# Optimization experiments

Hardware: AMD Instinct MI355X
Metric: run time of the kernel (lower is better)

The kernel has to match this reference:

```python
import jax, jax.numpy as jnp
import numpy as np
import math

N = 100000
E = 1600000
IN_DIM = 64
OUT_DIM = 64
EPS = 1e-5


def setup_inputs() -> dict:
    key = jax.random.key(0)
    ks = jax.random.split(key, 12)
    s = 1.0 / math.sqrt(IN_DIM)
    inp = {
        "geo_x": jax.random.normal(ks[0], (N, IN_DIM), dtype=jnp.float32),
        "euc_x": jax.random.normal(ks[1], (N, IN_DIM), dtype=jnp.float32),
        "Wq": jax.random.uniform(ks[2], (OUT_DIM, IN_DIM), minval=-s, maxval=s, dtype=jnp.float32),
        "bq": jnp.zeros((OUT_DIM,), jnp.float32),
        "Wk": jax.random.uniform(ks[3], (OUT_DIM, IN_DIM), minval=-s, maxval=s, dtype=jnp.float32),
        "bk": jnp.zeros((OUT_DIM,), jnp.float32),
        "Wv": jax.random.uniform(ks[4], (OUT_DIM, IN_DIM), minval=-s, maxval=s, dtype=jnp.float32),
        "bv": jnp.zeros((OUT_DIM,), jnp.float32),
        "Wskip": jax.random.uniform(ks[5], (OUT_DIM, IN_DIM), minval=-s, maxval=s, dtype=jnp.float32),
        "bskip": jnp.zeros((OUT_DIM,), jnp.float32),
        "ln_w": jnp.ones((OUT_DIM,), jnp.float32),
        "ln_b": jnp.zeros((OUT_DIM,), jnp.float32),
        "edge_index": jax.random.randint(ks[6], (2, E), 0, N, dtype=jnp.int64),
    }
    return inp


def reference(geo_x, euc_x, Wq, bq, Wk, bk, Wv, bv, Wskip, bskip, ln_w, ln_b, edge_index):
    n = euc_x.shape[0]
    src, dst = edge_index[0], edge_index[1]

    # TransformerConv, heads=1: q from target (euc), k/v from source (geo)
    q = euc_x @ Wq.T + bq                      # [N, C]
    k = geo_x @ Wk.T + bk                      # [N, C]
    v = geo_x @ Wv.T + bv                      # [N, C]
    C = q.shape[-1]

    # per-edge attention logits
    alpha = jnp.sum(q[dst] * k[src], axis=-1) / math.sqrt(C)   # [E]

    # segment softmax over incoming edges of each destination node
    amax = jax.ops.segment_max(alpha, dst, num_segments=n)
    amax = jnp.where(jnp.isfinite(amax), amax, 0.0)
    ex = jnp.exp(alpha - amax[dst])
    denom = jax.ops.segment_sum(ex, dst, num_segments=n)
    w = ex / (denom[dst] + 1e-16)                              # [E]

    # scatter-aggregate weighted values + root (skip) transform
    agg = jax.ops.segment_sum(w[:, None] * v[src], dst, num_segments=n)  # [N, C]
    out = agg + euc_x @ Wskip.T + bskip

    # PyG LayerNorm, mode='graph', batch=None: normalize over all nodes+channels
    mean = out.mean()
    xc = out - mean
    std = jnp.sqrt(jnp.mean(xc * xc))
    out = xc / (std + EPS) * ln_w + ln_b

    return jax.nn.relu(out)
```

## Files before the change

kernel.cpp:

```cpp
#include <hip/hip_runtime.h>
#include <hip/hip_fp16.h>


using short8 = __attribute__((ext_vector_type(8))) short;
using f32x4  = __attribute__((ext_vector_type(4))) float;
using h2     = __attribute__((ext_vector_type(2))) _Float16;
using u32x4  = __attribute__((ext_vector_type(4))) unsigned;
using u32x2  = __attribute__((ext_vector_type(2))) unsigned;
using f32x4v = __attribute__((ext_vector_type(4))) float;

#define QSCALE 31.75f
#define VDESC  0.031496062992f
#define SCI    1.7889250e-4f

#define CAP   4608
#define NCBMAX 400

__device__ inline int ntload(const int* p) {
    return __builtin_nontemporal_load(p);
}
__device__ inline unsigned ntload(const unsigned* p) {
    return __builtin_nontemporal_load(p);
}
__device__ inline uint2 ntload(const uint2* p) {
    u32x2 v = __builtin_nontemporal_load((const u32x2*)p);
    return make_uint2(v.x, v.y);
}
__device__ inline uint4 ntload(const uint4* p) {
    u32x4 v = __builtin_nontemporal_load((const u32x4*)p);
    return make_uint4(v.x, v.y, v.z, v.w);
}
__device__ inline float4 ntload(const float4* p) {
    f32x4v v = __builtin_nontemporal_load((const f32x4v*)p);
    return make_float4(v.x, v.y, v.z, v.w);
}
__device__ inline void ntstore(unsigned* p, unsigned v) {
    __builtin_nontemporal_store(v, p);
}
__device__ inline void ntstore(uint4* p, uint4 v) {
    u32x4 t; t.x = v.x; t.y = v.y; t.z = v.z; t.w = v.w;
    __builtin_nontemporal_store(t, (u32x4*)p);
}
__device__ inline void ntstore(float4* p, float4 v) {
    f32x4v t; t.x = v.x; t.y = v.y; t.z = v.z; t.w = v.w;
    __builtin_nontemporal_store(t, (f32x4v*)p);
}

__device__ inline unsigned short f2bf(float f) {
    unsigned u = __float_as_uint(f);
    unsigned r = u + 0x7FFFu + ((u >> 16) & 1u);
    return (unsigned short)(r >> 16);
}
__device__ inline unsigned short f2h(float f) {
    union { _Float16 h; unsigned short u; } c;
    c.h = (_Float16)f;
    return c.u;
}
__device__ inline h2 u2h2(unsigned u) {
    union { unsigned u; h2 h; } c; c.u = u; return c.h;
}
__device__ inline signed char f2i8(float f) {
    float v = f * QSCALE;
    v = fminf(fmaxf(v, -127.f), 127.f);
    return (signed char)__float2int_rn(v);
}

__device__ inline float fexp2(float x) {
#if __has_builtin(__builtin_amdgcn_exp2f)
    return __builtin_amdgcn_exp2f(x);
#else
    return __expf(x * 0.6931471805599453f);
#endif
}

__device__ inline int dot8i(uint2 q, uint2 k) {
#if __has_builtin(__builtin_amdgcn_sdot4)
    int t = __builtin_amdgcn_sdot4((int)q.x, (int)k.x, 0, false);
    return  __builtin_amdgcn_sdot4((int)q.y, (int)k.y, t, false);
#else
    int t = 0;
    #pragma unroll
    for (int i = 0; i < 4; ++i) {
        int qa = (int)(q.x << (24 - 8 * i)) >> 24;
        int ka = (int)(k.x << (24 - 8 * i)) >> 24;
        int qb = (int)(q.y << (24 - 8 * i)) >> 24;
        int kb = (int)(k.y << (24 - 8 * i)) >> 24;
        t += qa * ka + qb * kb;
    }
    return t;
#endif
}

__global__ __launch_bounds__(256) void k0_wconv(
    const float* __restrict__ Wq, const float* __restrict__ Wk,
    const float* __restrict__ Wv, const float* __restrict__ Wsk,
    unsigned short* __restrict__ wbf, int* __restrict__ zbase, int zcount)
{
    if (blockIdx.x == 16) {
        for (int i = threadIdx.x; i < zcount; i += 256) zbase[i] = 0;
        return;
    }
    int mat = blockIdx.x >> 2;
    int i4  = (blockIdx.x & 3) * 256 + threadIdx.x;
    const float* W = (mat == 0) ? Wq : (mat == 1) ? Wk : (mat == 2) ? Wv : Wsk;
    float4 w = *(const float4*)(W + (long)i4 * 4);
    ushort4 o;
    o.x = f2bf(w.x); o.y = f2bf(w.y); o.z = f2bf(w.z); o.w = f2bf(w.w);
    *(ushort4*)(wbf + (long)mat * 4096 + (long)i4 * 4) = o;
}

__global__ __launch_bounds__(256, 4) void k1_proj(
    const float* __restrict__ geo, const float* __restrict__ euc,
    const unsigned short* __restrict__ wbf,
    const float* __restrict__ bq, const float* __restrict__ bk,
    const float* __restrict__ bv, const float* __restrict__ bsk,
    signed char* __restrict__ q8b, signed char* __restrict__ kv8,
    unsigned short* __restrict__ skb, int N)
{
    __shared__ __align__(16) char smem[2 * 64 * 208];
    const int tid  = threadIdx.x;
    const int lane = tid & 63;
    const int w    = tid >> 6;
    const int qq   = lane >> 4;
    const int m    = lane & 15;
    const long base = (long)blockIdx.x * 128;

    char* t0 = smem;
    char* t1 = smem + 64 * 208;

    const long nodeA0 = base + w * 16 + m;
    const long nodeA1 = base + 64 + w * 16 + m;

    auto loadA = [&](const float* __restrict__ x, long node, short8 a[2]) {
        const float* px = x + node * 64;
        const bool v = (node < N);
        #pragma unroll
        for (int kh = 0; kh < 2; ++kh) {
            float4 f0 = v ? ntload((const float4*)(px + kh * 32 + qq * 8))
                          : make_float4(0.f, 0.f, 0.f, 0.f);
            float4 f1 = v ? ntload((const float4*)(px + kh * 32 + qq * 8 + 4))
                          : make_float4(0.f, 0.f, 0.f, 0.f);
            short8 r;
            r[0] = (short)f2bf(f0.x); r[1] = (short)f2bf(f0.y);
            r[2] = (short)f2bf(f0.z); r[3] = (short)f2bf(f0.w);
            r[4] = (short)f2bf(f1.x); r[5] = (short)f2bf(f1.y);
            r[6] = (short)f2bf(f1.z); r[7] = (short)f2bf(f1.w);
            a[kh] = r;
        }
    };
    auto loadB = [&](int mat, short8 b[2][4]) {
        #pragma unroll
        for (int kh = 0; kh < 2; ++kh)
            #pragma unroll
            for (int nt = 0; nt < 4; ++nt)
                b[kh][nt] = *(const short8*)(wbf + (long)mat * 4096 +
                                             (nt * 16 + m) * 64 + kh * 32 + qq * 8);
    };
    auto mmul = [&](const short8 a[2], const short8 b[2][4], f32x4 acc[4]) {
        #pragma unroll
        for (int nt = 0; nt < 4; ++nt) acc[nt] = (f32x4)(0.f);
        #pragma unroll
        for (int kh = 0; kh < 2; ++kh)
            #pragma unroll
            for (int nt = 0; nt < 4; ++nt)
                acc[nt] = __builtin_amdgcn_mfma_f32_16x16x32_bf16(a[kh], b[kh][nt], acc[nt], 0, 0, 0);
    };

    auto emit_i8 = [&](const f32x4 acc[4], const float* __restrict__ bias, char* tile) {
        #pragma unroll
        for (int nt = 0; nt < 4; ++nt) {
            int c = nt * 16 + m;
            float bs = bias[c];
            #pragma unroll
            for (int r = 0; r < 4; ++r) {
                int nl = w * 16 + qq * 4 + r;
                *(signed char*)(tile + nl * 208 + c) = f2i8(acc[nt][r] + bs);
            }
        }
    };
    auto emit_h = [&](const f32x4 acc[4], const float* __restrict__ bias, char* tile) {
        #pragma unroll
        for (int nt = 0; nt < 4; ++nt) {
            int c = nt * 16 + m;
            float bs = bias[c];
            #pragma unroll
            for (int r = 0; r < 4; ++r) {
                int nl = w * 16 + qq * 4 + r;
                *(unsigned short*)(tile + nl * 208 + 64 + c * 2) = f2h(acc[nt][r] + bs);
            }
        }
    };
    auto emit_kv = [&](const f32x4 acc[4], const float* __restrict__ bias,
                       char* tile, int vpart) {
        #pragma unroll
        for (int nt = 0; nt < 4; ++nt) {
            int c = nt * 16 + m;
            float bs = bias[c];
            int boff = (c >> 3) * 16 + vpart * 8 + (c & 7);
            #pragma unroll
            for (int r = 0; r < 4; ++r) {
                int nl = w * 16 + qq * 4 + r;
                *(signed char*)(tile + nl * 208 + boff) = f2i8(acc[nt][r] + bs);
            }
        }
    };

    short8 a0[2], a1[2];
    short8 B[2][4];
    f32x4 acc[4];

    loadA(euc, nodeA0, a0);
    loadA(euc, nodeA1, a1);
    loadB(0, B);
    mmul(a0, B, acc); emit_i8(acc, bq, t0);
    mmul(a1, B, acc); emit_i8(acc, bq, t1);
    loadB(3, B);
    mmul(a0, B, acc); emit_h(acc, bsk, t0);
    mmul(a1, B, acc); emit_h(acc, bsk, t1);
    __syncthreads();
    #pragma unroll
    for (int t = 0; t < 2; ++t) {
        const char* te = t ? t1 : t0;
        const long tb = base + t * 64;
        {
            int n = tid >> 2, j = tid & 3;
            long nd = tb + n;
            if (nd < N)
                *(int4*)(q8b + nd * 64 + j * 16) = *(const int4*)(te + n * 208 + j * 16);
        }
        #pragma unroll
        for (int it = 0; it < 2; ++it) {
            int idx = it * 256 + tid;
            int n = idx >> 3, j = idx & 7;
            long nd = tb + n;
            if (nd < N)
                *(int4*)((char*)skb + nd * 128 + j * 16) =
                    *(const int4*)(te + n * 208 + 64 + j * 16);
        }
    }
    __syncthreads();

    loadA(geo, nodeA0, a0);
    loadA(geo, nodeA1, a1);
    loadB(1, B);
    mmul(a0, B, acc); emit_kv(acc, bk, t0, 0);
    mmul(a1, B, acc); emit_kv(acc, bk, t1, 0);
    loadB(2, B);
    mmul(a0, B, acc); emit_kv(acc, bv, t0, 1);
    mmul(a1, B, acc); emit_kv(acc, bv, t1, 1);
    __syncthreads();
    #pragma unroll
    for (int t = 0; t < 2; ++t) {
        const char* tg = t ? t1 : t0;
        const long tb = base + t * 64;
        #pragma unroll
        for (int it = 0; it < 2; ++it) {
            int idx = it * 256 + tid;
            int n = idx >> 3, j = idx & 7;
            long nd = tb + n;
            if (nd < N)
                *(int4*)(kv8 + nd * 128 + j * 16) = *(const int4*)(tg + n * 208 + j * 16);
        }
    }
}

__global__ __launch_bounds__(512) void k2a_part(
    const int* __restrict__ ei, int E, int N,
    int* __restrict__ ccur, unsigned* __restrict__ tmp)
{
    __shared__ unsigned ebuf[4096];
    __shared__ unsigned short cbuf[4096];
    __shared__ int h[NCBMAX], offA[NCBMAX], lc[NCBMAX], creg[NCBMAX];
    __shared__ int sc[512];

    const int tid = threadIdx.x;
    const int NCB = (N + 255) >> 8;
    const long e0 = (long)blockIdx.x * 4096;
    const int tileN = (int)(((long)E - e0 < 4096) ? ((long)E - e0) : 4096);

    for (int i = tid; i < NCB; i += 512) { h[i] = 0; lc[i] = 0; }
    __syncthreads();

    const int* srcp = ei;
    const int* dstp = ei + E;
    unsigned wj[8];
    int cbj[8];
    #pragma unroll
    for (int j = 0; j < 8; ++j) {
        int i = j * 512 + tid;
        wj[j] = 0u; cbj[j] = -1;
        if (i < tileN) {
            int d = ntload(&dstp[e0 + i]), s = ntload(&srcp[e0 + i]);
            cbj[j] = d >> 8;
            wj[j]  = ((unsigned)(d & 255) << 17) | (unsigned)s;
            atomicAdd(&h[cbj[j]], 1);
        }
    }
    __syncthreads();

    sc[tid] = (tid < NCB) ? h[tid] : 0;
    __syncthreads();
    int own = sc[tid];
    for (int off = 1; off < 512; off <<= 1) {
        int v = (tid >= off) ? sc[tid - off] : 0;
        __syncthreads();
        sc[tid] += v;
        __syncthreads();
    }
    if (tid < NCB) offA[tid] = sc[tid] - own;
    if (tid < NCB && h[tid] > 0)
        creg[tid] = atomicAdd(&ccur[tid], h[tid]);
    __syncthreads();

    #pragma unroll
    for (int j = 0; j < 8; ++j) {
        if (cbj[j] >= 0) {
            int pos = offA[cbj[j]] + atomicAdd(&lc[cbj[j]], 1);
            ebuf[pos] = wj[j];
            cbuf[pos] = (unsigned short)cbj[j];
        }
    }
    __syncthreads();

    #pragma unroll
    for (int j = 0; j < 8; ++j) {
        int i = j * 512 + tid;
        if (i < tileN) {
            int cb = cbuf[i];
            int r  = creg[cb] + (i - offA[cb]);
            if (r < CAP) ntstore(&tmp[(long)cb * CAP + r], ebuf[i]);
        }
    }
}

__global__ __launch_bounds__(256, 8) void k3_attn(
    const signed char* __restrict__ q8b, const signed char* __restrict__ kv8,
    const unsigned short* __restrict__ skb,
    const int* __restrict__ ccnt, const unsigned* __restrict__ tmp,
    unsigned short* __restrict__ preb,
    float* __restrict__ partS, float* __restrict__ partSS, int N)
{
    __shared__ unsigned bkt[64 * 65];
    __shared__ int dcnt[64];
    __shared__ unsigned char perm[64];
    __shared__ float redS[4], redSS[4];
    const int tid  = threadIdx.x;
    const int lane = tid & 63;
    const int w    = tid >> 6;
    const int g0   = tid >> 3;
    const int gl   = tid & 7;
    const int bin  = blockIdx.x;
    const int cb   = bin >> 2;
    const unsigned sub = (unsigned)(bin & 3);
    const long nodeBase = (long)bin * 64;

    if (tid < 64) dcnt[tid] = 0;
    __syncthreads();

    int len = ccnt[cb];
    if (len > CAP) len = CAP;
    const unsigned* reg = tmp + (long)cb * CAP;
    for (int e = tid; e < len; e += 256) {
        unsigned wv = ntload(&reg[e]);
        if (((wv >> 23) & 3u) == sub) {
            int d = (wv >> 17) & 63;
            int slot = atomicAdd(&dcnt[d], 1);
            if (slot < 64) bkt[d * 65 + slot] = wv & 0x1FFFFu;
        }
    }
    __syncthreads();

    if (tid < 64) {
        int d = dcnt[tid]; if (d > 64) d = 64;
        int r = 0;
        for (int j = 0; j < 64; ++j) {
            int dj = dcnt[j]; if (dj > 64) dj = 64;
            r += (dj > d) || ((dj == d) && (j < tid));
        }
        perm[r] = (unsigned char)tid;
    }
    __syncthreads();

    float sacc = 0.f, ssacc = 0.f;

    for (int half = 0; half < 2; ++half) {
        const int row  = perm[half ? (63 - g0) : g0];
        const long node = nodeBase + row;

        uint2 qu = make_uint2(0, 0);
        if (node < N) qu = ntload((const uint2*)(q8b + node * 64 + gl * 8));

        int deg = dcnt[row];
        if (deg > 64) deg = 64;

        float den = 0.f;
        float a0=0.f,a1=0.f,a2=0.f,a3=0.f,a4=0.f,a5=0.f,a6=0.f,a7=0.f;

        auto vacc = [&](unsigned vx, unsigned vy, float ex) {
            a0 = fmaf((float)((int)(vx << 24) >> 24), ex, a0);
            a1 = fmaf((float)((int)(vx << 16) >> 24), ex, a1);
            a2 = fmaf((float)((int)(vx <<  8) >> 24), ex, a2);
            a3 = fmaf((float)((int)(vx      ) >> 24), ex, a3);
            a4 = fmaf((float)((int)(vy << 24) >> 24), ex, a4);
            a5 = fmaf((float)((int)(vy << 16) >> 24), ex, a5);
            a6 = fmaf((float)((int)(vy <<  8) >> 24), ex, a6);
            a7 = fmaf((float)((int)(vy      ) >> 24), ex, a7);
        };

        if (deg > 0) {
            const int rb  = row * 65;
            const int dm1 = deg - 1;
            auto ld = [&](int i) -> uint4 {
                int ii = (i < deg) ? i : dm1;
                unsigned s = bkt[rb + ii];
                return *(const uint4*)(kv8 + (long)s * 128 + gl * 16);
            };
            auto body = [&](uint4 r, int e) {
                int t = dot8i(qu, make_uint2(r.x, r.y));
                t += __shfl_xor(t, 1);
                t += __shfl_xor(t, 2);
                t += __shfl_xor(t, 4);
                float ex = (e < deg) ? fexp2((float)t * SCI) : 0.f;
                den += ex;
                vacc(r.z, r.w, ex);
            };

            uint4 r0 = ld(0), r1 = ld(1), r2 = ld(2), r3 = ld(3);
            for (int s = 0; s < deg; s += 4) {
                body(r0, s);     r0 = ld(s + 4);
                body(r1, s + 1); r1 = ld(s + 5);
                body(r2, s + 2); r2 = ld(s + 6);
                body(r3, s + 3); r3 = ld(s + 7);
            }
        }

        if (node < N) {
            float inv = VDESC / (den + 1e-16f);
            uint4 sk = ntload((const uint4*)((const char*)skb + node * 128 + gl * 16));
            h2 s0 = u2h2(sk.x), s1 = u2h2(sk.y), s2 = u2h2(sk.z), s3 = u2h2(sk.w);
            float o0 = a0 * inv + (float)s0.x, o1 = a1 * inv + (float)s0.y;
            float o2 = a2 * inv + (float)s1.x, o3 = a3 * inv + (float)s1.y;
            float o4 = a4 * inv + (float)s2.x, o5 = a5 * inv + (float)s2.y;
            float o6 = a6 * inv + (float)s3.x, o7 = a7 * inv + (float)s3.y;
            uint4 ov;
            ov.x = (unsigned)f2h(o0) | ((unsigned)f2h(o1) << 16);
            ov.y = (unsigned)f2h(o2) | ((unsigned)f2h(o3) << 16);
            ov.z = (unsigned)f2h(o4) | ((unsigned)f2h(o5) << 16);
            ov.w = (unsigned)f2h(o6) | ((unsigned)f2h(o7) << 16);
            ntstore((uint4*)((char*)preb + node * 128 + gl * 16), ov);
            sacc  += (o0 + o1 + o2 + o3) + (o4 + o5 + o6 + o7);
            ssacc += o0*o0 + o1*o1 + o2*o2 + o3*o3 + o4*o4 + o5*o5 + o6*o6 + o7*o7;
        }
    }

    #pragma unroll
    for (int m = 1; m <= 32; m <<= 1) {
        sacc  += __shfl_xor(sacc, m);
        ssacc += __shfl_xor(ssacc, m);
    }
    if (lane == 0) { redS[w] = sacc; redSS[w] = ssacc; }
    __syncthreads();
    if (tid == 0) {
        float s = 0.f, ss = 0.f;
        #pragma unroll
        for (int i = 0; i < 4; ++i) { s += redS[i]; ss += redSS[i]; }
        partS[bin]  = s;
        partSS[bin] = ss;
    }
}

__global__ __launch_bounds__(256) void k35_stats(
    const float* __restrict__ partS, const float* __restrict__ partSS,
    int nparts, float* __restrict__ stats, float M)
{
    __shared__ float rs[256], rss[256];
    float s = 0.f, ss = 0.f;
    for (int i = threadIdx.x; i < nparts; i += 256) { s += partS[i]; ss += partSS[i]; }
    rs[threadIdx.x] = s; rss[threadIdx.x] = ss;
    __syncthreads();
    for (int st = 128; st > 0; st >>= 1) {
        if (threadIdx.x < st) {
            rs[threadIdx.x]  += rs[threadIdx.x + st];
            rss[threadIdx.x] += rss[threadIdx.x + st];
        }
        __syncthreads();
    }
    if (threadIdx.x == 0) {
        float mean = rs[0] / M;
        float var  = rss[0] / M - mean * mean;
        if (var < 0.f) var = 0.f;
        stats[0] = mean;
        stats[1] = 1.f / (sqrtf(var) + 1e-5f);
    }
}

__global__ __launch_bounds__(256) void k4_ln(
    const unsigned short* __restrict__ preb, float* __restrict__ out,
    const float* __restrict__ lnw, const float* __restrict__ lnb,
    const float* __restrict__ stats, int M8)
{
    int i = blockIdx.x * 256 + threadIdx.x;
    if (i >= M8) return;
    float mean = stats[0], scale = stats[1];
    uint4 pv = ntload((const uint4*)((const char*)preb + (size_t)i * 16));
    int c8 = (i & 7) * 8;
    float4 w0 = *(const float4*)(lnw + c8);
    float4 w1 = *(const float4*)(lnw + c8 + 4);
    float4 b0 = *(const float4*)(lnb + c8);
    float4 b1 = *(const float4*)(lnb + c8 + 4);
    h2 p0 = u2h2(pv.x), p1 = u2h2(pv.y), p2 = u2h2(pv.z), p3 = u2h2(pv.w);
    float4 r0, r1;
    r0.x = fmaxf(((float)p0.x - mean) * scale * w0.x + b0.x, 0.f);
    r0.y = fmaxf(((float)p0.y - mean) * scale * w0.y + b0.y, 0.f);
    r0.z = fmaxf(((float)p1.x - mean) * scale * w0.z + b0.z, 0.f);
    r0.w = fmaxf(((float)p1.y - mean) * scale * w0.w + b0.w, 0.f);
    r1.x = fmaxf(((float)p2.x - mean) * scale * w1.x + b1.x, 0.f);
    r1.y = fmaxf(((float)p2.y - mean) * scale * w1.y + b1.y, 0.f);
    r1.z = fmaxf(((float)p3.x - mean) * scale * w1.z + b1.z, 0.f);
    r1.w = fmaxf(((float)p3.y - mean) * scale * w1.w + b1.w, 0.f);
    ntstore((float4*)(out + (size_t)i * 8), r0);
    ntstore((float4*)(out + (size_t)i * 8 + 4), r1);
}

extern "C" void kernel_launch(void* const* d_in, const int* in_sizes, int n_in,
                              void* d_out, int out_size, void* d_ws, size_t ws_size,
                              hipStream_t stream)
{
    const float* geo = (const float*)d_in[0];
    const float* euc = (const float*)d_in[1];
    const float* Wq  = (const float*)d_in[2];
    const float* bq  = (const float*)d_in[3];
    const float* Wk  = (const float*)d_in[4];
    const float* bk  = (const float*)d_in[5];
    const float* Wv  = (const float*)d_in[6];
    const float* bv  = (const float*)d_in[7];
    const float* Wsk = (const float*)d_in[8];
    const float* bsk = (const float*)d_in[9];
    const float* lnw = (const float*)d_in[10];
    const float* lnb = (const float*)d_in[11];
    const int*   ei  = (const int*)d_in[12];

    const int N = in_sizes[0] / 64;
    const int E = in_sizes[12] / 2;
    const int K = (N + 63) / 64;
    const int NCB = (N + 255) >> 8;
    float* out = (float*)d_out;

    char* p = (char*)d_ws;
    signed char*    q8b   = (signed char*)p;    p += (size_t)N * 64;
    signed char*    kv8   = (signed char*)p;    p += (size_t)N * 128;
    unsigned short* skb   = (unsigned short*)p; p += (size_t)N * 64 * 2;
    unsigned short* preb  = (unsigned short*)p; p += (size_t)N * 64 * 2;
    unsigned*       tmp   = (unsigned*)p;       p += (size_t)NCB * CAP * 4;
    unsigned short* wbf   = (unsigned short*)p; p += (size_t)4 * 4096 * 2;
    int* ccur = (int*)p;  p += (size_t)(NCB + 8) * 4;
    float* partS  = (float*)p; p += (size_t)K * 4;
    float* partSS = (float*)p; p += (size_t)K * 4;
    float* stats  = (float*)p;

    const int PB2 = (N + 127) / 128;

    k0_wconv<<<17, 256, 0, stream>>>(Wq, Wk, Wv, Wsk, wbf, ccur, NCB + 8);
    k1_proj<<<PB2, 256, 0, stream>>>(geo, euc, wbf, bq, bk, bv, bsk,
                                     q8b, kv8, skb, N);
    const int GA = (E + 4095) / 4096;
    k2a_part<<<GA, 512, 0, stream>>>(ei, E, N, ccur, tmp);
    k3_attn<<<K, 256, 0, stream>>>(q8b, kv8, skb, ccur, tmp, preb,
                                   partS, partSS, N);
    k35_stats<<<1, 256, 0, stream>>>(partS, partSS, K, stats, (float)N * 64.0f);
    const int M8 = N * 8;
    k4_ln<<<(M8 + 255) / 256, 256, 0, stream>>>(preb, out, lnw, lnb, stats, M8);
}
```

Before: 211.3 us.

## Fuse projection and edge partition kernels into one interleaved launch

Merges the node projection kernel and the edge bucketing kernel into a single 512-thread launch. Blocks are interleaved three at a time: two do projection tiles of 128 nodes and one partitions a 4096-edge tile. The two independent stages can then run concurrently on the GPU, and one launch and its inter-kernel gap go away. In exchange, the projection blocks now use 512 threads and shared memory sized for the partition path, which may change occupancy.

```diff
diff --git a/kernel.cpp b/kernel.cpp
--- a/kernel.cpp
+++ b/kernel.cpp
@@ -109,29 +109,107 @@
     *(ushort4*)(wbf + (long)mat * 4096 + (long)i4 * 4) = o;
 }
 
-__global__ __launch_bounds__(256, 4) void k1_proj(
+__global__ __launch_bounds__(512, 4) void k12_fused(
     const float* __restrict__ geo, const float* __restrict__ euc,
     const unsigned short* __restrict__ wbf,
     const float* __restrict__ bq, const float* __restrict__ bk,
     const float* __restrict__ bv, const float* __restrict__ bsk,
     signed char* __restrict__ q8b, signed char* __restrict__ kv8,
-    unsigned short* __restrict__ skb, int N)
+    unsigned short* __restrict__ skb,
+    const int* __restrict__ ei, int E,
+    int* __restrict__ ccur, unsigned* __restrict__ tmp,
+    int N, int R1, int GA)
 {
-    __shared__ __align__(16) char smem[2 * 64 * 208];
-    const int tid  = threadIdx.x;
-    const int lane = tid & 63;
-    const int w    = tid >> 6;
+    __shared__ __align__(16) char smem[33024];
+    const int tid = threadIdx.x;
+    const int g   = blockIdx.x / 3;
+    const int r   = blockIdx.x % 3;
+
+    if (r == 2) {
+        const int pid = g;
+        if (pid >= GA) return;
+        unsigned*       ebuf = (unsigned*)smem;
+        unsigned short* cbuf = (unsigned short*)(smem + 16384);
+        int* h    = (int*)(smem + 24576);
+        int* offA = (int*)(smem + 26176);
+        int* lc   = (int*)(smem + 27776);
+        int* creg = (int*)(smem + 29376);
+        int* sc   = (int*)(smem + 30976);
+
+        const int NCB = (N + 255) >> 8;
+        const long e0 = (long)pid * 4096;
+        const int tileN = (int)(((long)E - e0 < 4096) ? ((long)E - e0) : 4096);
+
+        for (int i = tid; i < NCB; i += 512) { h[i] = 0; lc[i] = 0; }
+        __syncthreads();
+
+        const int* srcp = ei;
+        const int* dstp = ei + E;
+        unsigned wj[8];
+        int cbj[8];
+        #pragma unroll
+        for (int j = 0; j < 8; ++j) {
+            int i = j * 512 + tid;
+            wj[j] = 0u; cbj[j] = -1;
+            if (i < tileN) {
+                int d = ntload(&dstp[e0 + i]), s = ntload(&srcp[e0 + i]);
+                cbj[j] = d >> 8;
+                wj[j]  = ((unsigned)(d & 255) << 17) | (unsigned)s;
+                atomicAdd(&h[cbj[j]], 1);
+            }
+        }
+        __syncthreads();
+
+        sc[tid] = (tid < NCB) ? h[tid] : 0;
+        __syncthreads();
+        int own = sc[tid];
+        for (int off = 1; off < 512; off <<= 1) {
+            int v = (tid >= off) ? sc[tid - off] : 0;
+            __syncthreads();
+            sc[tid] += v;
+            __syncthreads();
+        }
+        if (tid < NCB) offA[tid] = sc[tid] - own;
+        if (tid < NCB && h[tid] > 0)
+            creg[tid] = atomicAdd(&ccur[tid], h[tid]);
+        __syncthreads();
+
+        #pragma unroll
+        for (int j = 0; j < 8; ++j) {
+            if (cbj[j] >= 0) {
+                int pos = offA[cbj[j]] + atomicAdd(&lc[cbj[j]], 1);
+                ebuf[pos] = wj[j];
+                cbuf[pos] = (unsigned short)cbj[j];
+            }
+        }
+        __syncthreads();
+
+        #pragma unroll
+        for (int j = 0; j < 8; ++j) {
+            int i = j * 512 + tid;
+            if (i < tileN) {
+                int cb = cbuf[i];
+                int rr = creg[cb] + (i - offA[cb]);
+                if (rr < CAP) ntstore(&tmp[(long)cb * CAP + rr], ebuf[i]);
+            }
+        }
+        return;
+    }
+
+    const int kid = g * 2 + r;
+    if (kid >= R1) return;
+    const int t    = tid & 255;
+    const int half = tid >> 8;
+    const int lane = t & 63;
+    const int w    = t >> 6;
     const int qq   = lane >> 4;
     const int m    = lane & 15;
-    const long base = (long)blockIdx.x * 128;
-
-    char* t0 = smem;
-    char* t1 = smem + 64 * 208;
-
-    const long nodeA0 = base + w * 16 + m;
-    const long nodeA1 = base + 64 + w * 16 + m;
-
-    auto loadA = [&](const float* __restrict__ x, long node, short8 a[2]) {
+    const long tileBase = (long)kid * 128 + half * 64;
+
+    char* tile = smem + half * 13312;
+    const long node = tileBase + w * 16 + m;
+
+    auto loadA = [&](const float* __restrict__ x, short8 a[2]) {
         const float* px = x + node * 64;
         const bool v = (node < N);
         #pragma unroll
@@ -140,12 +218,12 @@
                           : make_float4(0.f, 0.f, 0.f, 0.f);
             float4 f1 = v ? ntload((const float4*)(px + kh * 32 + qq * 8 + 4))
                           : make_float4(0.f, 0.f, 0.f, 0.f);
-            short8 r;
-            r[0] = (short)f2bf(f0.x); r[1] = (short)f2bf(f0.y);
-            r[2] = (short)f2bf(f0.z); r[3] = (short)f2bf(f0.w);
-            r[4] = (short)f2bf(f1.x); r[5] = (short)f2bf(f1.y);
-            r[6] = (short)f2bf(f1.z); r[7] = (short)f2bf(f1.w);
-            a[kh] = r;
+            short8 rr;
+            rr[0] = (short)f2bf(f0.x); rr[1] = (short)f2bf(f0.y);
+            rr[2] = (short)f2bf(f0.z); rr[3] = (short)f2bf(f0.w);
+            rr[4] = (short)f2bf(f1.x); rr[5] = (short)f2bf(f1.y);
+            rr[6] = (short)f2bf(f1.z); rr[7] = (short)f2bf(f1.w);
+            a[kh] = rr;
         }
     };
     auto loadB = [&](int mat, short8 b[2][4]) {
@@ -166,170 +244,84 @@
                 acc[nt] = __builtin_amdgcn_mfma_f32_16x16x32_bf16(a[kh], b[kh][nt], acc[nt], 0, 0, 0);
     };
 
-    auto emit_i8 = [&](const f32x4 acc[4], const float* __restrict__ bias, char* tile) {
+    auto emit_i8 = [&](const f32x4 acc[4], const float* __restrict__ bias) {
         #pragma unroll
         for (int nt = 0; nt < 4; ++nt) {
             int c = nt * 16 + m;
             float bs = bias[c];
             #pragma unroll
-            for (int r = 0; r < 4; ++r) {
-                int nl = w * 16 + qq * 4 + r;
-                *(signed char*)(tile + nl * 208 + c) = f2i8(acc[nt][r] + bs);
+            for (int rr = 0; rr < 4; ++rr) {
+                int nl = w * 16 + qq * 4 + rr;
+                *(signed char*)(tile + nl * 208 + c) = f2i8(acc[nt][rr] + bs);
             }
         }
     };
-    auto emit_h = [&](const f32x4 acc[4], const float* __restrict__ bias, char* tile) {
+    auto emit_h = [&](const f32x4 acc[4], const float* __restrict__ bias) {
         #pragma unroll
         for (int nt = 0; nt < 4; ++nt) {
             int c = nt * 16 + m;
             float bs = bias[c];
             #pragma unroll
-            for (int r = 0; r < 4; ++r) {
-                int nl = w * 16 + qq * 4 + r;
-                *(unsigned short*)(tile + nl * 208 + 64 + c * 2) = f2h(acc[nt][r] + bs);
+            for (int rr = 0; rr < 4; ++rr) {
+                int nl = w * 16 + qq * 4 + rr;
+                *(unsigned short*)(tile + nl * 208 + 64 + c * 2) = f2h(acc[nt][rr] + bs);
             }
         }
     };
-    auto emit_kv = [&](const f32x4 acc[4], const float* __restrict__ bias,
-                       char* tile, int vpart) {
+    auto emit_kv = [&](const f32x4 acc[4], const float* __restrict__ bias, int vpart) {
         #pragma unroll
         for (int nt = 0; nt < 4; ++nt) {
             int c = nt * 16 + m;
             float bs = bias[c];
             int boff = (c >> 3) * 16 + vpart * 8 + (c & 7);
             #pragma unroll
-            for (int r = 0; r < 4; ++r) {
-                int nl = w * 16 + qq * 4 + r;
-                *(signed char*)(tile + nl * 208 + boff) = f2i8(acc[nt][r] + bs);
+            for (int rr = 0; rr < 4; ++rr) {
+                int nl = w * 16 + qq * 4 + rr;
+                *(signed char*)(tile + nl * 208 + boff) = f2i8(acc[nt][rr] + bs);
             }
         }
     };
 
-    short8 a0[2], a1[2];
+    short8 a[2];
     short8 B[2][4];
     f32x4 acc[4];
 
-    loadA(euc, nodeA0, a0);
-    loadA(euc, nodeA1, a1);
+    loadA(euc, a);
     loadB(0, B);
-    mmul(a0, B, acc); emit_i8(acc, bq, t0);
-    mmul(a1, B, acc); emit_i8(acc, bq, t1);
+    mmul(a, B, acc); emit_i8(acc, bq);
     loadB(3, B);
-    mmul(a0, B, acc); emit_h(acc, bsk, t0);
-    mmul(a1, B, acc); emit_h(acc, bsk, t1);
-    __syncthreads();
+    mmul(a, B, acc); emit_h(acc, bsk);
+    __syncthreads();
+    {
+        int n = t >> 2, j = t & 3;
+        long nd = tileBase + n;
+        if (nd < N)
+            *(int4*)(q8b + nd * 64 + j * 16) = *(const int4*)(tile + n * 208 + j * 16);
+    }
     #pragma unroll
-    for (int t = 0; t < 2; ++t) {
-        const char* te = t ? t1 : t0;
-        const long tb = base + t * 64;
-        {
-            int n = tid >> 2, j = tid & 3;
-            long nd = tb + n;
-            if (nd < N)
-                *(int4*)(q8b + nd * 64 + j * 16) = *(const int4*)(te + n * 208 + j * 16);
-        }
-        #pragma unroll
-        for (int it = 0; it < 2; ++it) {
-            int idx = it * 256 + tid;
-            int n = idx >> 3, j = idx & 7;
-            long nd = tb + n;
-            if (nd < N)
-                *(int4*)((char*)skb + nd * 128 + j * 16) =
-                    *(const int4*)(te + n * 208 + 64 + j * 16);
-        }
-    }
-    __syncthreads();
-
-    loadA(geo, nodeA0, a0);
-    loadA(geo, nodeA1, a1);
+    for (int it = 0; it < 2; ++it) {
+        int idx = it * 256 + t;
+        int n = idx >> 3, j = idx & 7;
+        long nd = tileBase + n;
+        if (nd < N)
+            *(int4*)((char*)skb + nd * 128 + j * 16) =
+                *(const int4*)(tile + n * 208 + 64 + j * 16);
+    }
+    __syncthreads();
+
+    loadA(geo, a);
     loadB(1, B);
-    mmul(a0, B, acc); emit_kv(acc, bk, t0, 0);
-    mmul(a1, B, acc); emit_kv(acc, bk, t1, 0);
+    mmul(a, B, acc); emit_kv(acc, bk, 0);
     loadB(2, B);
-    mmul(a0, B, acc); emit_kv(acc, bv, t0, 1);
-    mmul(a1, B, acc); emit_kv(acc, bv, t1, 1);
+    mmul(a, B, acc); emit_kv(acc, bv, 1);
     __syncthreads();
     #pragma unroll
-    for (int t = 0; t < 2; ++t) {
-        const char* tg = t ? t1 : t0;
-        const long tb = base + t * 64;
-        #pragma unroll
-        for (int it = 0; it < 2; ++it) {
-            int idx = it * 256 + tid;
-            int n = idx >> 3, j = idx & 7;
-            long nd = tb + n;
-            if (nd < N)
-                *(int4*)(kv8 + nd * 128 + j * 16) = *(const int4*)(tg + n * 208 + j * 16);
-        }
-    }
-}
-
-__global__ __launch_bounds__(512) void k2a_part(
-    const int* __restrict__ ei, int E, int N,
-    int* __restrict__ ccur, unsigned* __restrict__ tmp)
-{
-    __shared__ unsigned ebuf[4096];
-    __shared__ unsigned short cbuf[4096];
-    __shared__ int h[NCBMAX], offA[NCBMAX], lc[NCBMAX], creg[NCBMAX];
-    __shared__ int sc[512];
-
-    const int tid = threadIdx.x;
-    const int NCB = (N + 255) >> 8;
-    const long e0 = (long)blockIdx.x * 4096;
-    const int tileN = (int)(((long)E - e0 < 4096) ? ((long)E - e0) : 4096);
-
-    for (int i = tid; i < NCB; i += 512) { h[i] = 0; lc[i] = 0; }
-    __syncthreads();
-
-    const int* srcp = ei;
-    const int* dstp = ei + E;
-    unsigned wj[8];
-    int cbj[8];
-    #pragma unroll
-    for (int j = 0; j < 8; ++j) {
-        int i = j * 512 + tid;
-        wj[j] = 0u; cbj[j] = -1;
-        if (i < tileN) {
-            int d = ntload(&dstp[e0 + i]), s = ntload(&srcp[e0 + i]);
-            cbj[j] = d >> 8;
-            wj[j]  = ((unsigned)(d & 255) << 17) | (unsigned)s;
-            atomicAdd(&h[cbj[j]], 1);
-        }
-    }
-    __syncthreads();
-
-    sc[tid] = (tid < NCB) ? h[tid] : 0;
-    __syncthreads();
-    int own = sc[tid];
-    for (int off = 1; off < 512; off <<= 1) {
-        int v = (tid >= off) ? sc[tid - off] : 0;
-        __syncthreads();
-        sc[tid] += v;
-        __syncthreads();
-    }
-    if (tid < NCB) offA[tid] = sc[tid] - own;
-    if (tid < NCB && h[tid] > 0)
-        creg[tid] = atomicAdd(&ccur[tid], h[tid]);
-    __syncthreads();
-
-    #pragma unroll
-    for (int j = 0; j < 8; ++j) {
-        if (cbj[j] >= 0) {
-            int pos = offA[cbj[j]] + atomicAdd(&lc[cbj[j]], 1);
-            ebuf[pos] = wj[j];
-            cbuf[pos] = (unsigned short)cbj[j];
-        }
-    }
-    __syncthreads();
-
-    #pragma unroll
-    for (int j = 0; j < 8; ++j) {
-        int i = j * 512 + tid;
-        if (i < tileN) {
-            int cb = cbuf[i];
-            int r  = creg[cb] + (i - offA[cb]);
-            if (r < CAP) ntstore(&tmp[(long)cb * CAP + r], ebuf[i]);
-        }
+    for (int it = 0; it < 2; ++it) {
+        int idx = it * 256 + t;
+        int n = idx >> 3, j = idx & 7;
+        long nd = tileBase + n;
+        if (nd < N)
+            *(int4*)(kv8 + nd * 128 + j * 16) = *(const int4*)(tile + n * 208 + j * 16);
     }
 }
 
@@ -558,13 +550,14 @@
     float* partSS = (float*)p; p += (size_t)K * 4;
     float* stats  = (float*)p;
 
-    const int PB2 = (N + 127) / 128;
+    const int R1 = (N + 127) / 128;
+    const int GA = (E + 4095) / 4096;
+    const int G3 = ((R1 + 1) / 2 > GA) ? (R1 + 1) / 2 : GA;
 
     k0_wconv<<<17, 256, 0, stream>>>(Wq, Wk, Wv, Wsk, wbf, ccur, NCB + 8);
-    k1_proj<<<PB2, 256, 0, stream>>>(geo, euc, wbf, bq, bk, bv, bsk,
-                                     q8b, kv8, skb, N);
-    const int GA = (E + 4095) / 4096;
-    k2a_part<<<GA, 512, 0, stream>>>(ei, E, N, ccur, tmp);
+    k12_fused<<<3 * G3, 512, 0, stream>>>(geo, euc, wbf, bq, bk, bv, bsk,
+                                          q8b, kv8, skb, ei, E, ccur, tmp,
+                                          N, R1, GA);
     k3_attn<<<K, 256, 0, stream>>>(q8b, kv8, skb, ccur, tmp, preb,
                                    partS, partSS, N);
     k35_stats<<<1, 256, 0, stream>>>(partS, partSS, K, stats, (float)N * 64.0f);
```

Measured after the change: 213.4 us. About the same (+1.0%).
